# Performance work log

Hardware: AMD Instinct MI355X
Metric: run time of the kernel (lower is better)

## Reference

```python
import jax, jax.numpy as jnp
import numpy as np


def _feature_map(x):
    # elu(x) + 1, the canonical positive feature map for linear attention
    return jax.nn.elu(x) + 1.0


def setup_inputs() -> dict:
    key = jax.random.key(0)
    kq, kk, kv = jax.random.split(key, 3)
    B, T, H, D, M = 2, 2048, 8, 64, 64
    q = jax.random.normal(kq, (B, T, H, D), dtype=jnp.float32)
    k = jax.random.normal(kk, (B, T, H, D), dtype=jnp.float32)
    v = jax.random.normal(kv, (B, T, H, M), dtype=jnp.float32)
    return {"q": q, "k": k, "v": v}


def reference(q, k, v):
    # q,k: [B,T,H,D]; v: [B,T,H,M]
    qf = _feature_map(q)
    kf = _feature_map(k)
    # running sum of keys over time (causal)
    k_sum = jnp.cumsum(kf, axis=1)                      # [B,T,H,D]
    z = 1.0 / jnp.einsum('bthd,bthd->bth', qf, k_sum)   # [B,T,H]
    # outer products k_i v_i^T; NOTE: original torch code cumsums over dim=-2
    # (the D axis of the [B,T,H,D,M] tensor), reproduced faithfully here.
    kv = jnp.einsum('bthd,bthm->bthdm', kf, v)           # [B,T,H,D,M]
    kv_sum = jnp.cumsum(kv, axis=-2)                     # cumsum over D, per source
    out = jnp.einsum('bthd,bthdm,bth->bthm', qf, kv_sum, z)
    return out
```

## Files before the change

### kernel.cpp

```cpp
#include <hip/hip_runtime.h>
#include <hip/hip_bf16.h>

#define BB 2
#define TT 2048
#define HH 8
#define DD 64
#define CC 256
#define TC (TT / CC)
#define STRIDE (HH * DD)
#define NBH (BB * HH)
#define PW (CC / 16)

__device__ __forceinline__ float feat(float x) {
    return x > 0.f ? x + 1.f : __expf(x);
}


__global__ void __launch_bounds__(64)
chunk_sums_kernel(const float* __restrict__ k, float* __restrict__ ws) {
    const int idx  = blockIdx.x;
    const int c    = idx & (CC - 1);
    const int h    = (idx >> 8) & (HH - 1);
    const int b    = idx >> 11;
    const int lane = threadIdx.x;
    const int g    = lane & 15;
    const int seg  = lane >> 4;

    const size_t off0 = (((size_t)b * TT + c * TC + seg) * HH + h) * DD + g * 4;
    const float4 k0 = *(const float4*)(k + off0);
    const float4 k1 = *(const float4*)(k + off0 + (size_t)4 * STRIDE);

    float4 s;
    s.x = feat(k0.x) + feat(k1.x);
    s.y = feat(k0.y) + feat(k1.y);
    s.z = feat(k0.z) + feat(k1.z);
    s.w = feat(k0.w) + feat(k1.w);

    s.x += __shfl_xor(s.x, 16, 64); s.y += __shfl_xor(s.y, 16, 64);
    s.z += __shfl_xor(s.z, 16, 64); s.w += __shfl_xor(s.w, 16, 64);
    s.x += __shfl_xor(s.x, 32, 64); s.y += __shfl_xor(s.y, 32, 64);
    s.z += __shfl_xor(s.z, 32, 64); s.w += __shfl_xor(s.w, 32, 64);

    if (seg == 0)
        *(float4*)(ws + (size_t)idx * DD + g * 4) = s;
}

__global__ void __launch_bounds__(1024)
prefix_kernel(float* __restrict__ ws) {
    const int bh   = blockIdx.x;
    const int lane = threadIdx.x & 63;
    const int w    = threadIdx.x >> 6;

    size_t base = ((size_t)bh * CC + w * PW) * DD + lane;

    float val[PW];
    #pragma unroll
    for (int i = 0; i < PW; ++i) val[i] = ws[base + (size_t)i * DD];

    float run = 0.f, excl[PW];
    #pragma unroll
    for (int i = 0; i < PW; ++i) { excl[i] = run; run += val[i]; }

    __shared__ float tot[16][DD];
    tot[w][lane] = run;
    __syncthreads();

    float carry = 0.f;
    for (int w2 = 0; w2 < w; ++w2) carry += tot[w2][lane];

    #pragma unroll
    for (int i = 0; i < PW; ++i) ws[base + (size_t)i * DD] = excl[i] + carry;
}

__global__ void __launch_bounds__(64)
linattn_kernel(const float* __restrict__ q, const float* __restrict__ k,
               const float* __restrict__ v, const float* __restrict__ ws,
               float* __restrict__ out) {
    const int idx  = blockIdx.x;
    const int c    = idx & (CC - 1);
    const int h    = (idx >> 8) & (HH - 1);
    const int b    = idx >> 11;
    const int lane = threadIdx.x;
    const int g    = lane & 15;
    const int seg  = lane >> 4;

    const size_t off0 = (((size_t)b * TT + c * TC + seg) * HH + h) * DD + g * 4;
    const size_t off1 = off0 + (size_t)4 * STRIDE;

    float4 kf0 = *(const float4*)(k + off0);
    float4 kf1 = *(const float4*)(k + off1);
    float4 qf0 = *(const float4*)(q + off0);
    float4 qf1 = *(const float4*)(q + off1);
    const float4 vv0 = *(const float4*)(v + off0);
    const float4 vv1 = *(const float4*)(v + off1);
    const float4 carry = *(const float4*)(ws + (size_t)idx * DD + g * 4);

    kf0.x = feat(kf0.x); kf0.y = feat(kf0.y); kf0.z = feat(kf0.z); kf0.w = feat(kf0.w);
    kf1.x = feat(kf1.x); kf1.y = feat(kf1.y); kf1.z = feat(kf1.z); kf1.w = feat(kf1.w);
    qf0.x = feat(qf0.x); qf0.y = feat(qf0.y); qf0.z = feat(qf0.z); qf0.w = feat(qf0.w);
    qf1.x = feat(qf1.x); qf1.y = feat(qf1.y); qf1.z = feat(qf1.z); qf1.w = feat(qf1.w);

    float4 i0 = kf0, i1 = kf1;
    {
        float u;
        u = __shfl_up(i0.x, 16, 64); if (seg >= 1) i0.x += u;
        u = __shfl_up(i0.y, 16, 64); if (seg >= 1) i0.y += u;
        u = __shfl_up(i0.z, 16, 64); if (seg >= 1) i0.z += u;
        u = __shfl_up(i0.w, 16, 64); if (seg >= 1) i0.w += u;
        u = __shfl_up(i1.x, 16, 64); if (seg >= 1) i1.x += u;
        u = __shfl_up(i1.y, 16, 64); if (seg >= 1) i1.y += u;
        u = __shfl_up(i1.z, 16, 64); if (seg >= 1) i1.z += u;
        u = __shfl_up(i1.w, 16, 64); if (seg >= 1) i1.w += u;
        u = __shfl_up(i0.x, 32, 64); if (seg >= 2) i0.x += u;
        u = __shfl_up(i0.y, 32, 64); if (seg >= 2) i0.y += u;
        u = __shfl_up(i0.z, 32, 64); if (seg >= 2) i0.z += u;
        u = __shfl_up(i0.w, 32, 64); if (seg >= 2) i0.w += u;
        u = __shfl_up(i1.x, 32, 64); if (seg >= 2) i1.x += u;
        u = __shfl_up(i1.y, 32, 64); if (seg >= 2) i1.y += u;
        u = __shfl_up(i1.z, 32, 64); if (seg >= 2) i1.z += u;
        u = __shfl_up(i1.w, 32, 64); if (seg >= 2) i1.w += u;
    }
    float4 S0;
    S0.x = __shfl(i0.x, 48 + g, 64);
    S0.y = __shfl(i0.y, 48 + g, 64);
    S0.z = __shfl(i0.z, 48 + g, 64);
    S0.w = __shfl(i0.w, 48 + g, 64);

    float4 run0, run1;
    run0.x = carry.x + i0.x; run0.y = carry.y + i0.y;
    run0.z = carry.z + i0.z; run0.w = carry.w + i0.w;
    run1.x = carry.x + S0.x + i1.x; run1.y = carry.y + S0.y + i1.y;
    run1.z = carry.z + S0.z + i1.z; run1.w = carry.w + S0.w + i1.w;

    float4 p0, p1;
    p0.x = kf0.x; p0.y = p0.x + kf0.y; p0.z = p0.y + kf0.z; p0.w = p0.z + kf0.w;
    p1.x = kf1.x; p1.y = p1.x + kf1.y; p1.z = p1.y + kf1.z; p1.w = p1.z + kf1.w;
    float c0 = p0.w, c1 = p1.w;
    #pragma unroll
    for (int o = 1; o <= 8; o <<= 1) {
        float u0 = __shfl_up(c0, o, 16);
        float u1 = __shfl_up(c1, o, 16);
        if (g >= o) { c0 += u0; c1 += u1; }
    }
    const float e0 = c0 - p0.w;
    const float e1 = c1 - p1.w;
    float4 pre0, pre1;
    pre0.x = p0.x + e0; pre0.y = p0.y + e0; pre0.z = p0.z + e0; pre0.w = p0.w + e0;
    pre1.x = p1.x + e1; pre1.y = p1.y + e1; pre1.z = p1.z + e1; pre1.w = p1.w + e1;

    float s1_0 = qf0.x * pre0.x + qf0.y * pre0.y + qf0.z * pre0.z + qf0.w * pre0.w;
    float s2_0 = qf0.x * run0.x + qf0.y * run0.y + qf0.z * run0.z + qf0.w * run0.w;
    float s1_1 = qf1.x * pre1.x + qf1.y * pre1.y + qf1.z * pre1.z + qf1.w * pre1.w;
    float s2_1 = qf1.x * run1.x + qf1.y * run1.y + qf1.z * run1.z + qf1.w * run1.w;
    #pragma unroll
    for (int o = 1; o <= 8; o <<= 1) {
        s1_0 += __shfl_xor(s1_0, o, 64);
        s2_0 += __shfl_xor(s2_0, o, 64);
        s1_1 += __shfl_xor(s1_1, o, 64);
        s2_1 += __shfl_xor(s2_1, o, 64);
    }

    const float r0 = s1_0 / s2_0;
    const float r1 = s1_1 / s2_1;
    float4 o0, o1;
    o0.x = vv0.x * r0; o0.y = vv0.y * r0; o0.z = vv0.z * r0; o0.w = vv0.w * r0;
    o1.x = vv1.x * r1; o1.y = vv1.y * r1; o1.z = vv1.z * r1; o1.w = vv1.w * r1;
    *(float4*)(out + off0) = o0;
    *(float4*)(out + off1) = o1;
}

extern "C" void kernel_launch(void* const* d_in, const int* in_sizes, int n_in,
                              void* d_out, int out_size, void* d_ws, size_t ws_size,
                              hipStream_t stream) {
    const float* q = (const float*)d_in[0];
    const float* k = (const float*)d_in[1];
    const float* v = (const float*)d_in[2];
    float* out = (float*)d_out;
    float* ws  = (float*)d_ws;

    const int nblk = BB * HH * CC;
    chunk_sums_kernel<<<nblk, 64, 0, stream>>>(k, ws);
    prefix_kernel<<<NBH, 1024, 0, stream>>>(ws);
    linattn_kernel<<<nblk, 64, 0, stream>>>(q, k, v, ws, out);
}
```

Baseline: 80.34 us.

## Fuse chunk sums and prefix scan into one kernel with span totals

Merges the chunk-sum and prefix kernels into a single chunkscan kernel. Each 1024-thread block covers 16 chunks and scans them in shared memory, then writes per-chunk exclusive sums within the span plus one total per span. The final kernel adds up to 15 span totals to rebuild the global carry, which removes one kernel launch and one workspace round-trip at the cost of some redundant loads. The division is also replaced with a hardware reciprocal multiply, which is slightly less precise.

```diff
diff --git a/kernel.cpp b/kernel.cpp
--- a/kernel.cpp
+++ b/kernel.cpp
@@ -9,22 +9,29 @@
 #define TC (TT / CC)
 #define STRIDE (HH * DD)
 #define NBH (BB * HH)
-#define PW (CC / 16)
+#define NSPAN 16
+#define NCHUNK (NBH * CC)
 
 __device__ __forceinline__ float feat(float x) {
     return x > 0.f ? x + 1.f : __expf(x);
 }
 
 
-__global__ void __launch_bounds__(64)
-chunk_sums_kernel(const float* __restrict__ k, float* __restrict__ ws) {
-    const int idx  = blockIdx.x;
-    const int c    = idx & (CC - 1);
-    const int h    = (idx >> 8) & (HH - 1);
-    const int b    = idx >> 11;
-    const int lane = threadIdx.x;
+__global__ void __launch_bounds__(1024)
+chunkscan_kernel(const float* __restrict__ k, float* __restrict__ wse,
+                 float* __restrict__ wst) {
+    const int bh   = blockIdx.x >> 4;
+    const int span = blockIdx.x & (NSPAN - 1);
+    const int tid  = threadIdx.x;
+    const int w    = tid >> 6;
+    const int lane = tid & 63;
     const int g    = lane & 15;
     const int seg  = lane >> 4;
+
+    const int c   = span * NSPAN + w;
+    const int idx = bh * CC + c;
+    const int h   = bh & (HH - 1);
+    const int b   = bh >> 3;
 
     const size_t off0 = (((size_t)b * TT + c * TC + seg) * HH + h) * DD + g * 4;
     const float4 k0 = *(const float4*)(k + off0);
@@ -41,45 +48,36 @@
     s.x += __shfl_xor(s.x, 32, 64); s.y += __shfl_xor(s.y, 32, 64);
     s.z += __shfl_xor(s.z, 32, 64); s.w += __shfl_xor(s.w, 32, 64);
 
-    if (seg == 0)
-        *(float4*)(ws + (size_t)idx * DD + g * 4) = s;
-}
-
-__global__ void __launch_bounds__(1024)
-prefix_kernel(float* __restrict__ ws) {
-    const int bh   = blockIdx.x;
-    const int lane = threadIdx.x & 63;
-    const int w    = threadIdx.x >> 6;
-
-    size_t base = ((size_t)bh * CC + w * PW) * DD + lane;
-
-    float val[PW];
-    #pragma unroll
-    for (int i = 0; i < PW; ++i) val[i] = ws[base + (size_t)i * DD];
-
-    float run = 0.f, excl[PW];
-    #pragma unroll
-    for (int i = 0; i < PW; ++i) { excl[i] = run; run += val[i]; }
-
-    __shared__ float tot[16][DD];
-    tot[w][lane] = run;
+    __shared__ float tot[NSPAN][DD];
+    if (seg == 0) *(float4*)&tot[w][g * 4] = s;
     __syncthreads();
 
-    float carry = 0.f;
-    for (int w2 = 0; w2 < w; ++w2) carry += tot[w2][lane];
+    float4 carry = make_float4(0.f, 0.f, 0.f, 0.f);
+    for (int w2 = 0; w2 < w; ++w2) {
+        const float4 t = *(const float4*)&tot[w2][g * 4];
+        carry.x += t.x; carry.y += t.y; carry.z += t.z; carry.w += t.w;
+    }
 
-    #pragma unroll
-    for (int i = 0; i < PW; ++i) ws[base + (size_t)i * DD] = excl[i] + carry;
+    if (seg == 0) {
+        *(float4*)(wse + (size_t)idx * DD + g * 4) = carry;
+        if (w == NSPAN - 1) {
+            float4 t;
+            t.x = carry.x + s.x; t.y = carry.y + s.y;
+            t.z = carry.z + s.z; t.w = carry.w + s.w;
+            *(float4*)(wst + (size_t)(bh * NSPAN + span) * DD + g * 4) = t;
+        }
+    }
 }
 
 __global__ void __launch_bounds__(64)
 linattn_kernel(const float* __restrict__ q, const float* __restrict__ k,
-               const float* __restrict__ v, const float* __restrict__ ws,
-               float* __restrict__ out) {
+               const float* __restrict__ v, const float* __restrict__ wse,
+               const float* __restrict__ wst, float* __restrict__ out) {
     const int idx  = blockIdx.x;
     const int c    = idx & (CC - 1);
-    const int h    = (idx >> 8) & (HH - 1);
-    const int b    = idx >> 11;
+    const int bh   = idx >> 8;
+    const int h    = bh & (HH - 1);
+    const int b    = bh >> 3;
     const int lane = threadIdx.x;
     const int g    = lane & 15;
     const int seg  = lane >> 4;
@@ -93,7 +91,16 @@
     float4 qf1 = *(const float4*)(q + off1);
     const float4 vv0 = *(const float4*)(v + off0);
     const float4 vv1 = *(const float4*)(v + off1);
-    const float4 carry = *(const float4*)(ws + (size_t)idx * DD + g * 4);
+
+    float4 carry = *(const float4*)(wse + (size_t)idx * DD + g * 4);
+    {
+        const int span = c >> 4;
+        const float* wp = wst + (size_t)(bh * NSPAN) * DD + g * 4;
+        for (int s2 = 0; s2 < span; ++s2) {
+            const float4 t = *(const float4*)(wp + (size_t)s2 * DD);
+            carry.x += t.x; carry.y += t.y; carry.z += t.z; carry.w += t.w;
+        }
+    }
 
     kf0.x = feat(kf0.x); kf0.y = feat(kf0.y); kf0.z = feat(kf0.z); kf0.w = feat(kf0.w);
     kf1.x = feat(kf1.x); kf1.y = feat(kf1.y); kf1.z = feat(kf1.z); kf1.w = feat(kf1.w);
@@ -160,8 +167,8 @@
         s2_1 += __shfl_xor(s2_1, o, 64);
     }
 
-    const float r0 = s1_0 / s2_0;
-    const float r1 = s1_1 / s2_1;
+    const float r0 = s1_0 * __builtin_amdgcn_rcpf(s2_0);
+    const float r1 = s1_1 * __builtin_amdgcn_rcpf(s2_1);
     float4 o0, o1;
     o0.x = vv0.x * r0; o0.y = vv0.y * r0; o0.z = vv0.z * r0; o0.w = vv0.w * r0;
     o1.x = vv1.x * r1; o1.y = vv1.y * r1; o1.z = vv1.z * r1; o1.w = vv1.w * r1;
@@ -176,10 +183,9 @@
     const float* k = (const float*)d_in[1];
     const float* v = (const float*)d_in[2];
     float* out = (float*)d_out;
-    float* ws  = (float*)d_ws;
+    float* wse = (float*)d_ws;
+    float* wst = wse + (size_t)NCHUNK * DD;
 
-    const int nblk = BB * HH * CC;
-    chunk_sums_kernel<<<nblk, 64, 0, stream>>>(k, ws);
-    prefix_kernel<<<NBH, 1024, 0, stream>>>(ws);
-    linattn_kernel<<<nblk, 64, 0, stream>>>(q, k, v, ws, out);
+    chunkscan_kernel<<<NBH * NSPAN, 1024, 0, stream>>>(k, wse, wst);
+    linattn_kernel<<<NCHUNK, 64, 0, stream>>>(q, k, v, wse, wst, out);
 }
```

Measured after the change: 82.72 us. +3.0%, slower.
